# Kernel tuning notes

Measured on AMD Instinct MI355X. Metric: run time of the kernel, lower is better.

Reference implementation:

```python
import jax, jax.numpy as jnp
import numpy as np

N = 20000
E = 320000
HID = 256
NUM_RBF = 32
CUTOFF = 6.0
NUM_EDGE_TYPES = 2
LIGAND_NODE = 1
EPS = 1e-5

CENTERS = jnp.linspace(0.0, CUTOFF, NUM_RBF)  # [R]
GAMMA = 1.0 / max(float(CENTERS[1] - CENTERS[0]) ** 2, 1e-6)


def setup_inputs() -> dict:
    key = jax.random.key(0)
    ks = jax.random.split(key, 16)
    d = {}
    d['h'] = jax.random.normal(ks[0], (N, HID), dtype=jnp.float32)
    d['pos'] = jax.random.normal(ks[1], (N, 3), dtype=jnp.float32)
    d['edge_index'] = jax.random.randint(ks[2], (2, E), 0, N)
    d['edge_type'] = jax.random.randint(ks[3], (E,), 0, NUM_EDGE_TYPES)
    d['node_type'] = jax.random.randint(ks[4], (N,), 0, 2)
    s_in = 1.0 / np.sqrt(3 * HID + NUM_RBF)
    s_h = 1.0 / np.sqrt(HID)
    s_2h = 1.0 / np.sqrt(2 * HID)
    d['emb'] = jax.random.normal(ks[5], (NUM_EDGE_TYPES, HID), dtype=jnp.float32)
    d['W1m'] = jax.random.normal(ks[6], (3 * HID + NUM_RBF, HID), dtype=jnp.float32) * s_in
    d['b1m'] = jnp.zeros((HID,), dtype=jnp.float32)
    d['W2m'] = jax.random.normal(ks[7], (HID, HID), dtype=jnp.float32) * s_h
    d['b2m'] = jnp.zeros((HID,), dtype=jnp.float32)
    d['W1u'] = jax.random.normal(ks[8], (2 * HID, HID), dtype=jnp.float32) * s_2h
    d['b1u'] = jnp.zeros((HID,), dtype=jnp.float32)
    d['W2u'] = jax.random.normal(ks[9], (HID, HID), dtype=jnp.float32) * s_h
    d['b2u'] = jnp.zeros((HID,), dtype=jnp.float32)
    d['ln_g'] = jnp.ones((HID,), dtype=jnp.float32)
    d['ln_b'] = jnp.zeros((HID,), dtype=jnp.float32)
    return d


def _layernorm(x, g, b):
    mu = jnp.mean(x, axis=-1, keepdims=True)
    var = jnp.mean(jnp.square(x - mu), axis=-1, keepdims=True)
    return (x - mu) * jax.lax.rsqrt(var + EPS) * g + b


def reference(h, pos, edge_index, edge_type, node_type,
              emb, W1m, b1m, W2m, b2m, W1u, b1u, W2u, b2u, ln_g, ln_b):
    src, dst = edge_index[0], edge_index[1]
    rel = pos[src] - pos[dst]                      # [E,3]
    dist = jnp.linalg.norm(rel, axis=-1)           # [E]
    radial = jnp.exp(-GAMMA * jnp.square(dist[:, None] - CENTERS[None, :]))  # [E,R]
    edge_kind = emb[edge_type]                     # [E,H]
    m_in = jnp.concatenate([h[src], h[dst], edge_kind, radial], axis=-1)  # [E,3H+R]
    m = jax.nn.silu(m_in @ W1m + b1m)
    m_ij = jax.nn.silu(m @ W2m + b2m)              # [E,H] (dropout = identity in eval)
    seg_sum = jax.ops.segment_sum(m_ij, dst, num_segments=N)               # [N,H]
    cnt = jax.ops.segment_sum(jnp.ones((m_ij.shape[0],), m_ij.dtype), dst, num_segments=N)
    m_i = seg_sum / jnp.maximum(cnt, 1.0)[:, None]
    u = jax.nn.silu(jnp.concatenate([h, m_i], axis=-1) @ W1u + b1u)
    upd = u @ W2u + b2u                            # [N,H]
    lig = (node_type == LIGAND_NODE)[:, None]
    out = jnp.where(lig, _layernorm(h + upd, ln_g, ln_b), h)
    return out
```

## Files before the change

### kernel.cpp

```cpp
#include <hip/hip_runtime.h>
#include <hip/hip_fp16.h>
#include <math.h>

#define NN   20000
#define EE   320000
#define HID  256
#define GAMMA_C ((31.0f/6.0f)*(31.0f/6.0f))

typedef __attribute__((ext_vector_type(8)))  short    short8;
typedef __attribute__((ext_vector_type(8)))  _Float16 half8;
typedef __attribute__((ext_vector_type(16))) float    f32x16;

__device__ __forceinline__ float silu_f(float x) {
    return x / (1.0f + __expf(-x));
}

__device__ __forceinline__ short bf_hi(float x) {
    unsigned u = __float_as_uint(x);
    return (short)((u + 0x7fffu + ((u >> 16) & 1u)) >> 16);
}
__device__ __forceinline__ float bf_tof(short b) {
    return __uint_as_float(((unsigned)(unsigned short)b) << 16);
}
__device__ __forceinline__ void cvt_bf16_pair(float x, short* hi, short* lo) {
    short h = bf_hi(x);
    *hi = h;
    *lo = bf_hi(x - bf_tof(h));
}
__device__ __forceinline__ void cvt_f16_pair(float x, short* hi, short* lo) {
    __half h = __float2half_rn(x);
    *hi = (short)__half_as_ushort(h);
    *lo = (short)__half_as_ushort(__float2half_rn(x - __half2float(h)));
}
__device__ __forceinline__ short f16_bits(float x) {
    return (short)__half_as_ushort(__float2half_rn(x));
}

typedef __attribute__((address_space(1))) const void GV;
typedef __attribute__((address_space(3))) void LV;
__device__ __forceinline__ void gll16(const void* g, void* l) {
    __builtin_amdgcn_global_load_lds((GV*)g, (LV*)l, 16, 0, 0);
}

__device__ __forceinline__ short8 ldsfrag(const short* t, int row, int sg) {
    int s = sg ^ (row & 7);
    return *(const short8*)&t[row * 64 + s * 8];
}
__device__ __forceinline__ half8 ldsfragh(const short* t, int row, int sg) {
    int s = sg ^ (row & 7);
    return *(const half8*)&t[row * 64 + s * 8];
}

#define S0 (NN*HID)
#define S1 (2*HID)
#define S2 (256*800)
#define S3 (256*256)
#define S4 (256*512)
#define S5 (256*256)
#define PREP_TOTAL (S0+S1+S2+S3+S4+S5)

__global__ __launch_bounds__(256) void prep_all(
    const float* __restrict__ h, const float* __restrict__ emb,
    const float* __restrict__ W1m, const float* __restrict__ W2m,
    const float* __restrict__ W1u, const float* __restrict__ W2u,
    short* __restrict__ hpl, short* __restrict__ embpl,
    short* __restrict__ w1t, short* __restrict__ w2t,
    short* __restrict__ w1ut, short* __restrict__ w2ut)
{
    int i = blockIdx.x * 256 + threadIdx.x;
    float x; short *hi, *lo; int o; int f16 = 0;
    if (i < S0)              { x = h[i];   hi = hpl;   lo = hpl + S0;   o = i; }
    else if ((i -= S0) < S1) { x = emb[i]; hi = embpl; lo = embpl + S1; o = i; }
    else if ((i -= S1) < S2) { int n = i / 800, k = i - n * 800;
                               x = W1m[k * 256 + n]; hi = w1t; lo = w1t + S2; o = i; }
    else if ((i -= S2) < S3) { int n = i >> 8, k = i & 255;
                               x = W2m[k * 256 + n]; hi = w2t; lo = w2t + S3; o = i; f16 = 1; }
    else if ((i -= S3) < S4) { int n = i >> 9, k = i & 511;
                               x = W1u[k * 256 + n]; hi = w1ut; lo = w1ut + S4; o = i; }
    else if ((i -= S4) < S5) { int n = i >> 8, k = i & 255;
                               x = W2u[k * 256 + n]; hi = w2ut; lo = w2ut + S5; o = i; f16 = 1; }
    else return;
    short hb, lb;
    if (f16) cvt_f16_pair(x, &hb, &lb); else cvt_bf16_pair(x, &hb, &lb);
    hi[o] = hb; lo[o] = lb;
}

__global__ __launch_bounds__(512) void edge_mlp1(
    const short* __restrict__ hpl, const short* __restrict__ embpl,
    const short* __restrict__ w1t, const float* __restrict__ b1,
    const float* __restrict__ pos, const int* __restrict__ ei,
    const int* __restrict__ etype,
    short* __restrict__ mhi, float* __restrict__ cnt)
{
    __shared__ __align__(16) short At[128 * 64];
    __shared__ __align__(16) short Bt[256 * 64];
    __shared__ int srcS[128], dstS[128], etS[128];
    __shared__ float distS[128];

    const int tid = threadIdx.x, l = tid & 63, w = tid >> 6;
    const int e0 = blockIdx.x * 128;
    const int mh = w >> 2, ns = w & 3;

    if (tid < 128) {
        int s = ei[e0 + tid], d = ei[EE + e0 + tid];
        srcS[tid] = s; dstS[tid] = d; etS[tid] = etype[e0 + tid];
        float dx = pos[3*s]   - pos[3*d];
        float dy = pos[3*s+1] - pos[3*d+1];
        float dz = pos[3*s+2] - pos[3*d+2];
        distS[tid] = sqrtf(dx*dx + dy*dy + dz*dz);
        atomicAdd(&cnt[d], 1.0f);
    }
    __syncthreads();

    f32x16 acc[2][2];
    #pragma unroll
    for (int a = 0; a < 2; ++a)
        #pragma unroll
        for (int b = 0; b < 2; ++b)
            #pragma unroll
            for (int q = 0; q < 16; ++q) acc[a][b][q] = 0.0f;

    for (int c = 0; c < 25; ++c) {
        if (c < 24) {
            #pragma unroll
            for (int jj = 0; jj < 2; ++jj) {
                int j = w * 2 + jj;
                int row = j * 8 + (l >> 3), s = l & 7;
                int sg = s ^ (row & 7);
                int hl = sg >> 2, q = sg & 3;
                const short* gp;
                if (c < 8)
                    gp = hpl + (size_t)hl * (NN*HID) + (size_t)srcS[row] * HID + c*32 + q*8;
                else if (c < 16)
                    gp = hpl + (size_t)hl * (NN*HID) + (size_t)dstS[row] * HID + (c-8)*32 + q*8;
                else
                    gp = embpl + hl * (2*HID) + etS[row] * HID + (c-16)*32 + q*8;
                gll16(gp, &At[j * 512]);
            }
        } else {
            #pragma unroll
            for (int jj = 0; jj < 2; ++jj) {
                int it = tid * 2 + jj;
                int row = it >> 3, s = it & 7;
                int sg = s ^ (row & 7);
                int hl = sg >> 2, q = sg & 3;
                float d = distS[row];
                short8 v;
                #pragma unroll
                for (int k8 = 0; k8 < 8; ++k8) {
                    float cen = (float)(q * 8 + k8) * (6.0f / 31.0f);
                    float t = d - cen;
                    float f = __expf(-GAMMA_C * t * t);
                    short hb = bf_hi(f);
                    v[k8] = hl ? bf_hi(f - bf_tof(hb)) : hb;
                }
                *(short8*)&At[row * 64 + s * 8] = v;
            }
        }
        #pragma unroll
        for (int jj = 0; jj < 4; ++jj) {
            int j = w * 4 + jj;
            int n = j * 8 + (l >> 3), s = l & 7;
            int sg = s ^ (n & 7);
            int hl = sg >> 2, q = sg & 3;
            const short* gp = w1t + (size_t)hl * (256*800) + n * 800 + c*32 + q*8;
            gll16(gp, &Bt[j * 512]);
        }
        __syncthreads();
        #pragma unroll
        for (int t2 = 0; t2 < 2; ++t2) {
            short8 aF[2][2], bF[2][2];
            #pragma unroll
            for (int mf = 0; mf < 2; ++mf) {
                int row = mh * 64 + mf * 32 + (l & 31);
                #pragma unroll
                for (int hl = 0; hl < 2; ++hl)
                    aF[mf][hl] = ldsfrag(At, row, hl * 4 + t2 * 2 + (l >> 5));
            }
            #pragma unroll
            for (int nf = 0; nf < 2; ++nf) {
                int n = ns * 64 + nf * 32 + (l & 31);
                #pragma unroll
                for (int hl = 0; hl < 2; ++hl)
                    bF[nf][hl] = ldsfrag(Bt, n, hl * 4 + t2 * 2 + (l >> 5));
            }
            #pragma unroll
            for (int mf = 0; mf < 2; ++mf)
                #pragma unroll
                for (int nf = 0; nf < 2; ++nf) {
                    acc[mf][nf] = __builtin_amdgcn_mfma_f32_32x32x16_bf16(aF[mf][0], bF[nf][0], acc[mf][nf], 0, 0, 0);
                    acc[mf][nf] = __builtin_amdgcn_mfma_f32_32x32x16_bf16(aF[mf][0], bF[nf][1], acc[mf][nf], 0, 0, 0);
                    acc[mf][nf] = __builtin_amdgcn_mfma_f32_32x32x16_bf16(aF[mf][1], bF[nf][0], acc[mf][nf], 0, 0, 0);
                }
        }
        __syncthreads();
    }
    #pragma unroll
    for (int nf = 0; nf < 2; ++nf) {
        int col = ns * 64 + nf * 32 + (l & 31);
        float bb = b1[col];
        #pragma unroll
        for (int mf = 0; mf < 2; ++mf)
            #pragma unroll
            for (int r = 0; r < 16; ++r) {
                int row = mh * 64 + mf * 32 + (r & 3) + 8 * (r >> 2) + 4 * (l >> 5);
                float v = silu_f(acc[mf][nf][r] + bb);
                mhi[(size_t)(e0 + row) * HID + col] = f16_bits(v);
            }
    }
}

__global__ __launch_bounds__(512) void edge_mlp2(
    const short* __restrict__ mhi, const short* __restrict__ w2t,
    const float* __restrict__ b2, const int* __restrict__ ei,
    float* __restrict__ seg)
{
    __shared__ __align__(16) short Ah[128 * 64];
    __shared__ __align__(16) short Bh[256 * 64];
    __shared__ __align__(16) short Bl[256 * 64];
    __shared__ int dstS[128];
    const int tid = threadIdx.x, l = tid & 63, w = tid >> 6;
    const int e0 = blockIdx.x * 128;
    const int mh = w >> 2, ns = w & 3;
    if (tid < 128) dstS[tid] = ei[EE + e0 + tid];

    f32x16 acc[2][2];
    #pragma unroll
    for (int a = 0; a < 2; ++a)
        #pragma unroll
        for (int b = 0; b < 2; ++b)
            #pragma unroll
            for (int q = 0; q < 16; ++q) acc[a][b][q] = 0.0f;

    for (int c = 0; c < 4; ++c) {
        #pragma unroll
        for (int jj = 0; jj < 2; ++jj) {
            int j = w * 2 + jj;
            int row = j * 8 + (l >> 3), s = l & 7;
            int sg = s ^ (row & 7);
            gll16(mhi + (size_t)(e0 + row) * HID + c * 64 + sg * 8, &Ah[j * 512]);
        }
        #pragma unroll
        for (int jj = 0; jj < 8; ++jj) {
            int j = w * 8 + jj;
            int hf = j >> 5;
            int n = (j & 31) * 8 + (l >> 3), s = l & 7;
            int sg = s ^ (n & 7);
            const short* gp = w2t + (size_t)hf * (256*256) + n * HID + c * 64 + sg * 8;
            gll16(gp, hf ? &Bl[(j & 31) * 512] : &Bh[(j & 31) * 512]);
        }
        __syncthreads();
        #pragma unroll
        for (int t2 = 0; t2 < 4; ++t2) {
            int sg = t2 * 2 + (l >> 5);
            half8 aF[2], bH[2], bL[2];
            #pragma unroll
            for (int mf = 0; mf < 2; ++mf)
                aF[mf] = ldsfragh(Ah, mh * 64 + mf * 32 + (l & 31), sg);
            #pragma unroll
            for (int nf = 0; nf < 2; ++nf) {
                int n = ns * 64 + nf * 32 + (l & 31);
                bH[nf] = ldsfragh(Bh, n, sg);
                bL[nf] = ldsfragh(Bl, n, sg);
            }
            #pragma unroll
            for (int mf = 0; mf < 2; ++mf)
                #pragma unroll
                for (int nf = 0; nf < 2; ++nf) {
                    acc[mf][nf] = __builtin_amdgcn_mfma_f32_32x32x16_f16(aF[mf], bH[nf], acc[mf][nf], 0, 0, 0);
                    acc[mf][nf] = __builtin_amdgcn_mfma_f32_32x32x16_f16(aF[mf], bL[nf], acc[mf][nf], 0, 0, 0);
                }
        }
        __syncthreads();
    }
    #pragma unroll
    for (int nf = 0; nf < 2; ++nf) {
        int col = ns * 64 + nf * 32 + (l & 31);
        float bb = b2[col];
        #pragma unroll
        for (int mf = 0; mf < 2; ++mf)
            #pragma unroll
            for (int r = 0; r < 16; ++r) {
                int row = mh * 64 + mf * 32 + (r & 3) + 8 * (r >> 2) + 4 * (l >> 5);
                float v = silu_f(acc[mf][nf][r] + bb);
                atomicAdd(&seg[(size_t)dstS[row] * HID + col], v);
            }
    }
}

__global__ __launch_bounds__(256) void mi_prep(
    const float* __restrict__ seg, const float* __restrict__ cnt,
    short* __restrict__ mipl)
{
    int i = blockIdx.x * 256 + threadIdx.x;
    int row = i >> 8;
    float v = seg[i] / fmaxf(cnt[row], 1.0f);
    short hb, lb;
    cvt_bf16_pair(v, &hb, &lb);
    mipl[i] = hb;
    mipl[(size_t)NN * HID + i] = lb;
}

__global__ __launch_bounds__(512) void node_mlp1(
    const short* __restrict__ hpl, const short* __restrict__ mipl,
    const short* __restrict__ w1ut, const float* __restrict__ b1,
    short* __restrict__ u)
{
    __shared__ __align__(16) short At[128 * 64];
    __shared__ __align__(16) short Bt[256 * 64];
    const int tid = threadIdx.x, l = tid & 63, w = tid >> 6;
    const int n0 = blockIdx.x * 128;
    const int mh = w >> 2, ns = w & 3;

    f32x16 acc[2][2];
    #pragma unroll
    for (int a = 0; a < 2; ++a)
        #pragma unroll
        for (int b = 0; b < 2; ++b)
            #pragma unroll
            for (int q = 0; q < 16; ++q) acc[a][b][q] = 0.0f;

    for (int c = 0; c < 16; ++c) {
        #pragma unroll
        for (int jj = 0; jj < 2; ++jj) {
            int j = w * 2 + jj;
            int row = j * 8 + (l >> 3), s = l & 7;
            int sg = s ^ (row & 7);
            int hl = sg >> 2, q = sg & 3;
            int node = min(n0 + row, NN - 1);
            const short* gp = (c < 8)
                ? hpl  + (size_t)hl * (NN*HID) + (size_t)node * HID + c * 32 + q * 8
                : mipl + (size_t)hl * (NN*HID) + (size_t)node * HID + (c - 8) * 32 + q * 8;
            gll16(gp, &At[j * 512]);
        }
        #pragma unroll
        for (int jj = 0; jj < 4; ++jj) {
            int j = w * 4 + jj;
            int n = j * 8 + (l >> 3), s = l & 7;
            int sg = s ^ (n & 7);
            int hl = sg >> 2, q = sg & 3;
            const short* gp = w1ut + (size_t)hl * (256*512) + n * 512 + c * 32 + q * 8;
            gll16(gp, &Bt[j * 512]);
        }
        __syncthreads();
        #pragma unroll
        for (int t2 = 0; t2 < 2; ++t2) {
            short8 aF[2][2], bF[2][2];
            #pragma unroll
            for (int mf = 0; mf < 2; ++mf) {
                int row = mh * 64 + mf * 32 + (l & 31);
                #pragma unroll
                for (int hl = 0; hl < 2; ++hl)
                    aF[mf][hl] = ldsfrag(At, row, hl * 4 + t2 * 2 + (l >> 5));
            }
            #pragma unroll
            for (int nf = 0; nf < 2; ++nf) {
                int n = ns * 64 + nf * 32 + (l & 31);
                #pragma unroll
                for (int hl = 0; hl < 2; ++hl)
                    bF[nf][hl] = ldsfrag(Bt, n, hl * 4 + t2 * 2 + (l >> 5));
            }
            #pragma unroll
            for (int mf = 0; mf < 2; ++mf)
                #pragma unroll
                for (int nf = 0; nf < 2; ++nf) {
                    acc[mf][nf] = __builtin_amdgcn_mfma_f32_32x32x16_bf16(aF[mf][0], bF[nf][0], acc[mf][nf], 0, 0, 0);
                    acc[mf][nf] = __builtin_amdgcn_mfma_f32_32x32x16_bf16(aF[mf][0], bF[nf][1], acc[mf][nf], 0, 0, 0);
                    acc[mf][nf] = __builtin_amdgcn_mfma_f32_32x32x16_bf16(aF[mf][1], bF[nf][0], acc[mf][nf], 0, 0, 0);
                }
        }
        __syncthreads();
    }
    #pragma unroll
    for (int nf = 0; nf < 2; ++nf) {
        int col = ns * 64 + nf * 32 + (l & 31);
        float bb = b1[col];
        #pragma unroll
        for (int mf = 0; mf < 2; ++mf)
            #pragma unroll
            for (int r = 0; r < 16; ++r) {
                int row = mh * 64 + mf * 32 + (r & 3) + 8 * (r >> 2) + 4 * (l >> 5);
                if (n0 + row < NN) {
                    float v = silu_f(acc[mf][nf][r] + bb);
                    u[(size_t)(n0 + row) * HID + col] = f16_bits(v);
                }
            }
    }
}

__global__ __launch_bounds__(512) void node_mlp2(
    const short* __restrict__ u, const short* __restrict__ w2ut,
    const float* __restrict__ b2, const float* __restrict__ h,
    const int* __restrict__ ntype, const float* __restrict__ lng,
    const float* __restrict__ lnb, float* __restrict__ out)
{
    __shared__ __align__(16) short Ah[128 * 64];
    __shared__ __align__(16) short Bh[256 * 64];
    __shared__ __align__(16) short Bl[256 * 64];
    __shared__ float red1[4][128], red2[4][128];
    __shared__ float muS[128], rsS[128];
    const int tid = threadIdx.x, l = tid & 63, w = tid >> 6;
    const int n0 = blockIdx.x * 128;
    const int mh = w >> 2, ns = w & 3;

    f32x16 acc[2][2];
    #pragma unroll
    for (int a = 0; a < 2; ++a)
        #pragma unroll
        for (int b = 0; b < 2; ++b)
            #pragma unroll
            for (int q = 0; q < 16; ++q) acc[a][b][q] = 0.0f;

    for (int c = 0; c < 4; ++c) {
        #pragma unroll
        for (int jj = 0; jj < 2; ++jj) {
            int j = w * 2 + jj;
            int row = j * 8 + (l >> 3), s = l & 7;
            int sg = s ^ (row & 7);
            int node = min(n0 + row, NN - 1);
            gll16(u + (size_t)node * HID + c * 64 + sg * 8, &Ah[j * 512]);
        }
        #pragma unroll
        for (int jj = 0; jj < 8; ++jj) {
            int j = w * 8 + jj;
            int hf = j >> 5;
            int n = (j & 31) * 8 + (l >> 3), s = l & 7;
            int sg = s ^ (n & 7);
            const short* gp = w2ut + (size_t)hf * (256*256) + n * HID + c * 64 + sg * 8;
            gll16(gp, hf ? &Bl[(j & 31) * 512] : &Bh[(j & 31) * 512]);
        }
        __syncthreads();
        #pragma unroll
        for (int t2 = 0; t2 < 4; ++t2) {
            int sg = t2 * 2 + (l >> 5);
            half8 aF[2], bH[2], bL[2];
            #pragma unroll
            for (int mf = 0; mf < 2; ++mf)
                aF[mf] = ldsfragh(Ah, mh * 64 + mf * 32 + (l & 31), sg);
            #pragma unroll
            for (int nf = 0; nf < 2; ++nf) {
                int n = ns * 64 + nf * 32 + (l & 31);
                bH[nf] = ldsfragh(Bh, n, sg);
                bL[nf] = ldsfragh(Bl, n, sg);
            }
            #pragma unroll
            for (int mf = 0; mf < 2; ++mf)
                #pragma unroll
                for (int nf = 0; nf < 2; ++nf) {
                    acc[mf][nf] = __builtin_amdgcn_mfma_f32_32x32x16_f16(aF[mf], bH[nf], acc[mf][nf], 0, 0, 0);
                    acc[mf][nf] = __builtin_amdgcn_mfma_f32_32x32x16_f16(aF[mf], bL[nf], acc[mf][nf], 0, 0, 0);
                }
        }
        __syncthreads();
    }

    #pragma unroll
    for (int nf = 0; nf < 2; ++nf) {
        int col = ns * 64 + nf * 32 + (l & 31);
        float bb = b2[col];
        #pragma unroll
        for (int mf = 0; mf < 2; ++mf)
            #pragma unroll
            for (int r = 0; r < 16; ++r) {
                int row = mh * 64 + mf * 32 + (r & 3) + 8 * (r >> 2) + 4 * (l >> 5);
                int node = min(n0 + row, NN - 1);
                acc[mf][nf][r] += bb + h[(size_t)node * HID + col];
            }
    }
    #pragma unroll
    for (int mf = 0; mf < 2; ++mf)
        #pragma unroll
        for (int r = 0; r < 16; ++r) {
            float v1 = acc[mf][0][r] + acc[mf][1][r];
            float v2 = acc[mf][0][r]*acc[mf][0][r] + acc[mf][1][r]*acc[mf][1][r];
            #pragma unroll
            for (int off = 16; off >= 1; off >>= 1) {
                v1 += __shfl_xor(v1, off, 64);
                v2 += __shfl_xor(v2, off, 64);
            }
            if ((l & 31) == 0) {
                int row = mh * 64 + mf * 32 + (r & 3) + 8 * (r >> 2) + 4 * (l >> 5);
                red1[ns][row] = v1; red2[ns][row] = v2;
            }
        }
    __syncthreads();
    if (tid < 128) {
        float s1 = red1[0][tid] + red1[1][tid] + red1[2][tid] + red1[3][tid];
        float s2 = red2[0][tid] + red2[1][tid] + red2[2][tid] + red2[3][tid];
        float mu = s1 * (1.0f / 256.0f);
        float var = s2 * (1.0f / 256.0f) - mu * mu;
        muS[tid] = mu;
        rsS[tid] = rsqrtf(var + 1e-5f);
    }
    __syncthreads();
    #pragma unroll
    for (int nf = 0; nf < 2; ++nf) {
        int col = ns * 64 + nf * 32 + (l & 31);
        float g = lng[col], bt = lnb[col];
        #pragma unroll
        for (int mf = 0; mf < 2; ++mf)
            #pragma unroll
            for (int r = 0; r < 16; ++r) {
                int row = mh * 64 + mf * 32 + (r & 3) + 8 * (r >> 2) + 4 * (l >> 5);
                int node = n0 + row;
                if (node < NN) {
                    float y;
                    if (ntype[node] == 1)
                        y = (acc[mf][nf][r] - muS[row]) * rsS[row] * g + bt;
                    else
                        y = h[(size_t)node * HID + col];
                    out[(size_t)node * HID + col] = y;
                }
            }
    }
}

#define SWZ(k, e) ((e) ^ ((((k) >> 2) & 7) << 2))

__global__ __launch_bounds__(256) void edge_fp32(
    const float* __restrict__ h, const float* __restrict__ pos,
    const int* __restrict__ ei, const int* __restrict__ etype,
    const float* __restrict__ emb,
    const float* __restrict__ W1, const float* __restrict__ b1,
    const float* __restrict__ W2, const float* __restrict__ b2,
    float* __restrict__ seg, float* __restrict__ cnt)
{
    __shared__ float A1T[16][32];
    __shared__ float Bt[16][256];
    __shared__ float A2T[256][32];
    __shared__ float distS[32];
    __shared__ int   srcS[32], dstS[32], etS[32];
    const int tid = threadIdx.x;
    const int e0  = blockIdx.x * 32;
    if (tid < 32) {
        const int e = e0 + tid;
        const int s = ei[e];
        const int d = ei[EE + e];
        srcS[tid] = s; dstS[tid] = d; etS[tid] = etype[e];
        const float dx = pos[3*s+0] - pos[3*d+0];
        const float dy = pos[3*s+1] - pos[3*d+1];
        const float dz = pos[3*s+2] - pos[3*d+2];
        distS[tid] = sqrtf(dx*dx + dy*dy + dz*dz);
        atomicAdd(&cnt[d], 1.0f);
    }
    __syncthreads();
    const int c0 = (tid & 63) * 4;
    const int r0 = (tid >> 6) * 8;
    float acc[8][4];
    #pragma unroll
    for (int i = 0; i < 8; ++i)
        #pragma unroll
        for (int j = 0; j < 4; ++j) acc[i][j] = 0.0f;
    const float step  = 6.0f / 31.0f;
    for (int k0 = 0; k0 < 800; k0 += 16) {
        if (tid < 128) {
            const int e = tid >> 2;
            const int q = (tid & 3) * 4;
            const int k = k0 + q;
            float4 v;
            if (k < 256)       v = *(const float4*)&h[(size_t)srcS[e]*HID + k];
            else if (k < 512)  v = *(const float4*)&h[(size_t)dstS[e]*HID + (k - 256)];
            else if (k < 768)  v = *(const float4*)&emb[(size_t)etS[e]*HID + (k - 512)];
            else {
                const float de = distS[e];
                const float t0 = de - step*(float)(k-768);
                const float t1 = de - step*(float)(k-767);
                const float t2 = de - step*(float)(k-766);
                const float t3 = de - step*(float)(k-765);
                v = make_float4(__expf(-GAMMA_C*t0*t0), __expf(-GAMMA_C*t1*t1),
                                __expf(-GAMMA_C*t2*t2), __expf(-GAMMA_C*t3*t3));
            }
            A1T[q+0][e] = v.x; A1T[q+1][e] = v.y;
            A1T[q+2][e] = v.z; A1T[q+3][e] = v.w;
        }
        #pragma unroll
        for (int p = 0; p < 4; ++p) {
            const int idx = p*256 + tid;
            const int k   = idx >> 6;
            const int n   = (idx & 63) * 4;
            *(float4*)&Bt[k][n] = *(const float4*)&W1[(size_t)(k0+k)*HID + n];
        }
        __syncthreads();
        #pragma unroll
        for (int kk = 0; kk < 16; ++kk) {
            const float4 b  = *(const float4*)&Bt[kk][c0];
            const float4 a0 = *(const float4*)&A1T[kk][r0];
            const float4 a1 = *(const float4*)&A1T[kk][r0+4];
            const float a[8] = {a0.x,a0.y,a0.z,a0.w,a1.x,a1.y,a1.z,a1.w};
            #pragma unroll
            for (int i = 0; i < 8; ++i) {
                acc[i][0] = fmaf(a[i], b.x, acc[i][0]);
                acc[i][1] = fmaf(a[i], b.y, acc[i][1]);
                acc[i][2] = fmaf(a[i], b.z, acc[i][2]);
                acc[i][3] = fmaf(a[i], b.w, acc[i][3]);
            }
        }
        __syncthreads();
    }
    {
        const float4 b1v = *(const float4*)&b1[c0];
        const float bb[4] = {b1v.x, b1v.y, b1v.z, b1v.w};
        #pragma unroll
        for (int j = 0; j < 4; ++j) {
            const int k = c0 + j;
            #pragma unroll
            for (int i = 0; i < 8; ++i) {
                const float x = acc[i][j] + bb[j];
                A2T[k][SWZ(k, r0+i)] = silu_f(x);
                acc[i][j] = 0.0f;
            }
        }
    }
    __syncthreads();
    for (int k0 = 0; k0 < HID; k0 += 16) {
        #pragma unroll
        for (int p = 0; p < 4; ++p) {
            const int idx = p*256 + tid;
            const int k   = idx >> 6;
            const int n   = (idx & 63) * 4;
            *(float4*)&Bt[k][n] = *(const float4*)&W2[(size_t)(k0+k)*HID + n];
        }
        __syncthreads();
        #pragma unroll
        for (int kk = 0; kk < 16; ++kk) {
            const int K = k0 + kk;
            const float4 b  = *(const float4*)&Bt[kk][c0];
            const float4 a0 = *(const float4*)&A2T[K][SWZ(K, r0)];
            const float4 a1 = *(const float4*)&A2T[K][SWZ(K, r0+4)];
            const float a[8] = {a0.x,a0.y,a0.z,a0.w,a1.x,a1.y,a1.z,a1.w};
            #pragma unroll
            for (int i = 0; i < 8; ++i) {
                acc[i][0] = fmaf(a[i], b.x, acc[i][0]);
                acc[i][1] = fmaf(a[i], b.y, acc[i][1]);
                acc[i][2] = fmaf(a[i], b.z, acc[i][2]);
                acc[i][3] = fmaf(a[i], b.w, acc[i][3]);
            }
        }
        __syncthreads();
    }
    {
        const float4 b2v = *(const float4*)&b2[c0];
        const float bb[4] = {b2v.x, b2v.y, b2v.z, b2v.w};
        #pragma unroll
        for (int i = 0; i < 8; ++i) {
            const int d = dstS[r0 + i];
            float* outp = &seg[(size_t)d*HID + c0];
            #pragma unroll
            for (int j = 0; j < 4; ++j) {
                const float x = acc[i][j] + bb[j];
                atomicAdd(&outp[j], silu_f(x));
            }
        }
    }
}

__global__ __launch_bounds__(256) void node_fp32(
    const float* __restrict__ h, const float* __restrict__ seg,
    const float* __restrict__ cnt, const int* __restrict__ ntype,
    const float* __restrict__ W1, const float* __restrict__ b1,
    const float* __restrict__ W2, const float* __restrict__ b2,
    const float* __restrict__ lng, const float* __restrict__ lnb,
    float* __restrict__ out)
{
    __shared__ float A1T[16][32];
    __shared__ float Bt[16][256];
    __shared__ float A2T[256][32];
    __shared__ float invS[32];
    const int tid = threadIdx.x;
    const int n0  = blockIdx.x * 32;
    if (tid < 32) invS[tid] = 1.0f / fmaxf(cnt[n0 + tid], 1.0f);
    __syncthreads();
    const int c0 = (tid & 63) * 4;
    const int r0 = (tid >> 6) * 8;
    float acc[8][4];
    #pragma unroll
    for (int i = 0; i < 8; ++i)
        #pragma unroll
        for (int j = 0; j < 4; ++j) acc[i][j] = 0.0f;
    for (int k0 = 0; k0 < 512; k0 += 16) {
        if (tid < 128) {
            const int e = tid >> 2;
            const int q = (tid & 3) * 4;
            const int k = k0 + q;
            float4 v;
            if (k < 256) v = *(const float4*)&h[(size_t)(n0+e)*HID + k];
            else {
                v = *(const float4*)&seg[(size_t)(n0+e)*HID + (k - 256)];
                const float ic = invS[e];
                v.x *= ic; v.y *= ic; v.z *= ic; v.w *= ic;
            }
            A1T[q+0][e] = v.x; A1T[q+1][e] = v.y;
            A1T[q+2][e] = v.z; A1T[q+3][e] = v.w;
        }
        #pragma unroll
        for (int p = 0; p < 4; ++p) {
            const int idx = p*256 + tid;
            const int k   = idx >> 6;
            const int n   = (idx & 63) * 4;
            *(float4*)&Bt[k][n] = *(const float4*)&W1[(size_t)(k0+k)*HID + n];
        }
        __syncthreads();
        #pragma unroll
        for (int kk = 0; kk < 16; ++kk) {
            const float4 b  = *(const float4*)&Bt[kk][c0];
            const float4 a0 = *(const float4*)&A1T[kk][r0];
            const float4 a1 = *(const float4*)&A1T[kk][r0+4];
            const float a[8] = {a0.x,a0.y,a0.z,a0.w,a1.x,a1.y,a1.z,a1.w};
            #pragma unroll
            for (int i = 0; i < 8; ++i) {
                acc[i][0] = fmaf(a[i], b.x, acc[i][0]);
                acc[i][1] = fmaf(a[i], b.y, acc[i][1]);
                acc[i][2] = fmaf(a[i], b.z, acc[i][2]);
                acc[i][3] = fmaf(a[i], b.w, acc[i][3]);
            }
        }
        __syncthreads();
    }
    {
        const float4 b1v = *(const float4*)&b1[c0];
        const float bb[4] = {b1v.x, b1v.y, b1v.z, b1v.w};
        #pragma unroll
        for (int j = 0; j < 4; ++j) {
            const int k = c0 + j;
            #pragma unroll
            for (int i = 0; i < 8; ++i) {
                const float x = acc[i][j] + bb[j];
                A2T[k][SWZ(k, r0+i)] = silu_f(x);
                acc[i][j] = 0.0f;
            }
        }
    }
    __syncthreads();
    for (int k0 = 0; k0 < HID; k0 += 16) {
        #pragma unroll
        for (int p = 0; p < 4; ++p) {
            const int idx = p*256 + tid;
            const int k   = idx >> 6;
            const int n   = (idx & 63) * 4;
            *(float4*)&Bt[k][n] = *(const float4*)&W2[(size_t)(k0+k)*HID + n];
        }
        __syncthreads();
        #pragma unroll
        for (int kk = 0; kk < 16; ++kk) {
            const int K = k0 + kk;
            const float4 b  = *(const float4*)&Bt[kk][c0];
            const float4 a0 = *(const float4*)&A2T[K][SWZ(K, r0)];
            const float4 a1 = *(const float4*)&A2T[K][SWZ(K, r0+4)];
            const float a[8] = {a0.x,a0.y,a0.z,a0.w,a1.x,a1.y,a1.z,a1.w};
            #pragma unroll
            for (int i = 0; i < 8; ++i) {
                acc[i][0] = fmaf(a[i], b.x, acc[i][0]);
                acc[i][1] = fmaf(a[i], b.y, acc[i][1]);
                acc[i][2] = fmaf(a[i], b.z, acc[i][2]);
                acc[i][3] = fmaf(a[i], b.w, acc[i][3]);
            }
        }
        __syncthreads();
    }
    {
        const float4 b2v = *(const float4*)&b2[c0];
        const float bb[4] = {b2v.x, b2v.y, b2v.z, b2v.w};
        float4 hv[8];
        #pragma unroll
        for (int i = 0; i < 8; ++i) {
            hv[i] = *(const float4*)&h[(size_t)(n0+r0+i)*HID + c0];
            acc[i][0] = hv[i].x + acc[i][0] + bb[0];
            acc[i][1] = hv[i].y + acc[i][1] + bb[1];
            acc[i][2] = hv[i].z + acc[i][2] + bb[2];
            acc[i][3] = hv[i].w + acc[i][3] + bb[3];
        }
        float s1[8], s2[8];
        #pragma unroll
        for (int i = 0; i < 8; ++i) {
            s1[i] = acc[i][0] + acc[i][1] + acc[i][2] + acc[i][3];
            s2[i] = acc[i][0]*acc[i][0] + acc[i][1]*acc[i][1]
                  + acc[i][2]*acc[i][2] + acc[i][3]*acc[i][3];
        }
        #pragma unroll
        for (int off = 32; off >= 1; off >>= 1) {
            #pragma unroll
            for (int i = 0; i < 8; ++i) {
                s1[i] += __shfl_xor(s1[i], off, 64);
                s2[i] += __shfl_xor(s2[i], off, 64);
            }
        }
        const float4 gv = *(const float4*)&lng[c0];
        const float4 bv = *(const float4*)&lnb[c0];
        const float g[4] = {gv.x, gv.y, gv.z, gv.w};
        const float bb2[4] = {bv.x, bv.y, bv.z, bv.w};
        #pragma unroll
        for (int i = 0; i < 8; ++i) {
            const int n = n0 + r0 + i;
            const bool lig = (ntype[n] == 1);
            float4 y;
            if (lig) {
                const float mu  = s1[i] * (1.0f/256.0f);
                const float var = s2[i] * (1.0f/256.0f) - mu*mu;
                const float rs  = rsqrtf(var + 1e-5f);
                y.x = (acc[i][0] - mu) * rs * g[0] + bb2[0];
                y.y = (acc[i][1] - mu) * rs * g[1] + bb2[1];
                y.z = (acc[i][2] - mu) * rs * g[2] + bb2[2];
                y.w = (acc[i][3] - mu) * rs * g[3] + bb2[3];
            } else {
                y = hv[i];
            }
            *(float4*)&out[(size_t)n*HID + c0] = y;
        }
    }
}

extern "C" void kernel_launch(void* const* d_in, const int* in_sizes, int n_in,
                              void* d_out, int out_size, void* d_ws, size_t ws_size,
                              hipStream_t stream) {
    (void)in_sizes; (void)n_in; (void)out_size;
    const float* h    = (const float*)d_in[0];
    const float* pos  = (const float*)d_in[1];
    const int*   ei   = (const int*)  d_in[2];
    const int*   et   = (const int*)  d_in[3];
    const int*   nt   = (const int*)  d_in[4];
    const float* emb  = (const float*)d_in[5];
    const float* W1m  = (const float*)d_in[6];
    const float* b1m  = (const float*)d_in[7];
    const float* W2m  = (const float*)d_in[8];
    const float* b2m  = (const float*)d_in[9];
    const float* W1u  = (const float*)d_in[10];
    const float* b1u  = (const float*)d_in[11];
    const float* W2u  = (const float*)d_in[12];
    const float* b2u  = (const float*)d_in[13];
    const float* lng  = (const float*)d_in[14];
    const float* lnb  = (const float*)d_in[15];
    float* out = (float*)d_out;

    size_t o = 0;
    auto al = [&](size_t b) { size_t r = o; o = (o + b + 511) & ~(size_t)511; return r; };
    const size_t o_seg  = al((size_t)NN * HID * 4);
    const size_t o_cnt  = al((size_t)NN * 4);
    const size_t o_zend = o;
    const size_t o_hpl  = al((size_t)2 * NN * HID * 2);
    const size_t o_emb  = al((size_t)2 * 2 * HID * 2);
    const size_t o_w1t  = al((size_t)2 * 256 * 800 * 2);
    const size_t o_w2t  = al((size_t)2 * 256 * 256 * 2);
    const size_t o_w1ut = al((size_t)2 * 256 * 512 * 2);
    const size_t o_w2ut = al((size_t)2 * 256 * 256 * 2);
    const size_t o_mipl = al((size_t)2 * NN * HID * 2);
    const size_t o_upl  = al((size_t)NN * HID * 2);
    const size_t o_mhi  = al((size_t)EE * HID * 2);
    const size_t need = o;

    char* ws = (char*)d_ws;
    float* seg = (float*)(ws + o_seg);
    float* cnt = (float*)(ws + o_cnt);

    if (ws_size >= need) {
        short* hpl   = (short*)(ws + o_hpl);
        short* embpl = (short*)(ws + o_emb);
        short* w1t   = (short*)(ws + o_w1t);
        short* w2t   = (short*)(ws + o_w2t);
        short* w1ut  = (short*)(ws + o_w1ut);
        short* w2ut  = (short*)(ws + o_w2ut);
        short* mipl  = (short*)(ws + o_mipl);
        short* upl   = (short*)(ws + o_upl);
        short* mhi   = (short*)(ws + o_mhi);

        hipMemsetAsync(d_ws, 0, o_zend, stream);
        prep_all<<<PREP_TOTAL / 256, 256, 0, stream>>>(
            h, emb, W1m, W2m, W1u, W2u, hpl, embpl, w1t, w2t, w1ut, w2ut);
        edge_mlp1<<<EE / 128, 512, 0, stream>>>(
            hpl, embpl, w1t, b1m, pos, ei, et, mhi, cnt);
        edge_mlp2<<<EE / 128, 512, 0, stream>>>(mhi, w2t, b2m, ei, seg);
        mi_prep<<<(NN * HID) / 256, 256, 0, stream>>>(seg, cnt, mipl);
        const int nb = (NN + 127) / 128;
        node_mlp1<<<nb, 512, 0, stream>>>(hpl, mipl, w1ut, b1u, upl);
        node_mlp2<<<nb, 512, 0, stream>>>(upl, w2ut, b2u, h, nt, lng, lnb, out);
    } else {
        hipMemsetAsync(d_ws, 0, ((size_t)NN * HID + NN) * sizeof(float), stream);
        float* seg0 = (float*)d_ws;
        float* cnt0 = seg0 + (size_t)NN * HID;
        edge_fp32<<<EE / 32, 256, 0, stream>>>(h, pos, ei, et, emb,
                                               W1m, b1m, W2m, b2m, seg0, cnt0);
        node_fp32<<<NN / 32, 256, 0, stream>>>(h, seg0, cnt0, nt,
                                               W1u, b1u, W2u, b2u, lng, lnb, out);
    }
}
```

Baseline: 1.015 ms.

## Split edge MLP output columns across grid and double-buffer LDS tiles

Both edge MLP kernels now split the 256 output columns into two 128-column halves via blockIdx.y, which doubles the number of blocks. Each block keeps smaller LDS tiles, double-buffered so the next K-chunk is loaded while the current one feeds the MFMAs. Launch bounds request 4 blocks per CU to raise occupancy and hide gather latency. In exchange, the gathered A rows (h[src], h[dst], emb, and the radial features) are loaded and computed twice, once per column half.

```diff
diff --git a/kernel.cpp b/kernel.cpp
--- a/kernel.cpp
+++ b/kernel.cpp
@@ -45,6 +45,14 @@
 __device__ __forceinline__ short8 ldsfrag(const short* t, int row, int sg) {
     int s = sg ^ (row & 7);
     return *(const short8*)&t[row * 64 + s * 8];
+}
+__device__ __forceinline__ half8 ldsfragh32(const short* t, int row, int sg) {
+    int s = sg ^ (row & 3);
+    return *(const half8*)&t[row * 32 + s * 8];
+}
+__device__ __forceinline__ short8 ldsfrag32(const short* t, int row, int sg) {
+    int s = sg ^ (row & 3);
+    return *(const short8*)&t[row * 32 + s * 8];
 }
 __device__ __forceinline__ half8 ldsfragh(const short* t, int row, int sg) {
     int s = sg ^ (row & 7);
@@ -85,20 +93,21 @@
     hi[o] = hb; lo[o] = lb;
 }
 
-__global__ __launch_bounds__(512) void edge_mlp1(
+__global__ __launch_bounds__(512, 4) void edge_mlp1(
     const short* __restrict__ hpl, const short* __restrict__ embpl,
     const short* __restrict__ w1t, const float* __restrict__ b1,
     const float* __restrict__ pos, const int* __restrict__ ei,
     const int* __restrict__ etype,
     short* __restrict__ mhi, float* __restrict__ cnt)
 {
-    __shared__ __align__(16) short At[128 * 64];
-    __shared__ __align__(16) short Bt[256 * 64];
+    __shared__ __align__(16) short At[2][128 * 64];
+    __shared__ __align__(16) short Bt[2][128 * 64];
     __shared__ int srcS[128], dstS[128], etS[128];
     __shared__ float distS[128];
 
     const int tid = threadIdx.x, l = tid & 63, w = tid >> 6;
     const int e0 = blockIdx.x * 128;
+    const int cb = blockIdx.y;
     const int mh = w >> 2, ns = w & 3;
 
     if (tid < 128) {
@@ -108,19 +117,11 @@
         float dy = pos[3*s+1] - pos[3*d+1];
         float dz = pos[3*s+2] - pos[3*d+2];
         distS[tid] = sqrtf(dx*dx + dy*dy + dz*dz);
-        atomicAdd(&cnt[d], 1.0f);
+        if (cb == 0) atomicAdd(&cnt[d], 1.0f);
     }
     __syncthreads();
 
-    f32x16 acc[2][2];
-    #pragma unroll
-    for (int a = 0; a < 2; ++a)
-        #pragma unroll
-        for (int b = 0; b < 2; ++b)
-            #pragma unroll
-            for (int q = 0; q < 16; ++q) acc[a][b][q] = 0.0f;
-
-    for (int c = 0; c < 25; ++c) {
+    auto stageA = [&](int buf, int c) {
         if (c < 24) {
             #pragma unroll
             for (int jj = 0; jj < 2; ++jj) {
@@ -135,7 +136,7 @@
                     gp = hpl + (size_t)hl * (NN*HID) + (size_t)dstS[row] * HID + (c-8)*32 + q*8;
                 else
                     gp = embpl + hl * (2*HID) + etS[row] * HID + (c-16)*32 + q*8;
-                gll16(gp, &At[j * 512]);
+                gll16(gp, &At[buf][j * 512]);
             }
         } else {
             #pragma unroll
@@ -154,135 +155,153 @@
                     short hb = bf_hi(f);
                     v[k8] = hl ? bf_hi(f - bf_tof(hb)) : hb;
                 }
-                *(short8*)&At[row * 64 + s * 8] = v;
-            }
-        }
-        #pragma unroll
-        for (int jj = 0; jj < 4; ++jj) {
-            int j = w * 4 + jj;
+                *(short8*)&At[buf][row * 64 + s * 8] = v;
+            }
+        }
+    };
+    auto stageB = [&](int buf, int c) {
+        #pragma unroll
+        for (int jj = 0; jj < 2; ++jj) {
+            int j = w * 2 + jj;
             int n = j * 8 + (l >> 3), s = l & 7;
             int sg = s ^ (n & 7);
             int hl = sg >> 2, q = sg & 3;
-            const short* gp = w1t + (size_t)hl * (256*800) + n * 800 + c*32 + q*8;
-            gll16(gp, &Bt[j * 512]);
-        }
-        __syncthreads();
+            const short* gp = w1t + (size_t)hl * (256*800)
+                            + (size_t)(cb*128 + n) * 800 + c*32 + q*8;
+            gll16(gp, &Bt[buf][j * 512]);
+        }
+    };
+
+    f32x16 acc[2];
+    #pragma unroll
+    for (int a = 0; a < 2; ++a)
+        #pragma unroll
+        for (int q = 0; q < 16; ++q) acc[a][q] = 0.0f;
+
+    stageA(0, 0); stageB(0, 0);
+    __syncthreads();
+
+    int cur = 0;
+    for (int c = 0; c < 25; ++c) {
+        if (c < 24) { stageA(cur ^ 1, c + 1); stageB(cur ^ 1, c + 1); }
         #pragma unroll
         for (int t2 = 0; t2 < 2; ++t2) {
-            short8 aF[2][2], bF[2][2];
+            short8 aF[2][2], bF[2];
             #pragma unroll
             for (int mf = 0; mf < 2; ++mf) {
                 int row = mh * 64 + mf * 32 + (l & 31);
                 #pragma unroll
                 for (int hl = 0; hl < 2; ++hl)
-                    aF[mf][hl] = ldsfrag(At, row, hl * 4 + t2 * 2 + (l >> 5));
-            }
-            #pragma unroll
-            for (int nf = 0; nf < 2; ++nf) {
-                int n = ns * 64 + nf * 32 + (l & 31);
+                    aF[mf][hl] = ldsfrag(&At[cur][0], row, hl * 4 + t2 * 2 + (l >> 5));
+            }
+            {
+                int n = ns * 32 + (l & 31);
                 #pragma unroll
                 for (int hl = 0; hl < 2; ++hl)
-                    bF[nf][hl] = ldsfrag(Bt, n, hl * 4 + t2 * 2 + (l >> 5));
-            }
-            #pragma unroll
-            for (int mf = 0; mf < 2; ++mf)
-                #pragma unroll
-                for (int nf = 0; nf < 2; ++nf) {
-                    acc[mf][nf] = __builtin_amdgcn_mfma_f32_32x32x16_bf16(aF[mf][0], bF[nf][0], acc[mf][nf], 0, 0, 0);
-                    acc[mf][nf] = __builtin_amdgcn_mfma_f32_32x32x16_bf16(aF[mf][0], bF[nf][1], acc[mf][nf], 0, 0, 0);
-                    acc[mf][nf] = __builtin_amdgcn_mfma_f32_32x32x16_bf16(aF[mf][1], bF[nf][0], acc[mf][nf], 0, 0, 0);
-                }
-        }
-        __syncthreads();
-    }
-    #pragma unroll
-    for (int nf = 0; nf < 2; ++nf) {
-        int col = ns * 64 + nf * 32 + (l & 31);
+                    bF[hl] = ldsfrag(&Bt[cur][0], n, hl * 4 + t2 * 2 + (l >> 5));
+            }
+            #pragma unroll
+            for (int mf = 0; mf < 2; ++mf) {
+                acc[mf] = __builtin_amdgcn_mfma_f32_32x32x16_bf16(aF[mf][0], bF[0], acc[mf], 0, 0, 0);
+                acc[mf] = __builtin_amdgcn_mfma_f32_32x32x16_bf16(aF[mf][0], bF[1], acc[mf], 0, 0, 0);
+                acc[mf] = __builtin_amdgcn_mfma_f32_32x32x16_bf16(aF[mf][1], bF[0], acc[mf], 0, 0, 0);
+            }
+        }
+        __syncthreads();
+        cur ^= 1;
+    }
+
+    {
+        int col = cb * 128 + ns * 32 + (l & 31);
         float bb = b1[col];
         #pragma unroll
         for (int mf = 0; mf < 2; ++mf)
             #pragma unroll
             for (int r = 0; r < 16; ++r) {
                 int row = mh * 64 + mf * 32 + (r & 3) + 8 * (r >> 2) + 4 * (l >> 5);
-                float v = silu_f(acc[mf][nf][r] + bb);
+                float v = silu_f(acc[mf][r] + bb);
                 mhi[(size_t)(e0 + row) * HID + col] = f16_bits(v);
             }
     }
 }
 
-__global__ __launch_bounds__(512) void edge_mlp2(
+__global__ __launch_bounds__(512, 4) void edge_mlp2(
     const short* __restrict__ mhi, const short* __restrict__ w2t,
     const float* __restrict__ b2, const int* __restrict__ ei,
     float* __restrict__ seg)
 {
-    __shared__ __align__(16) short Ah[128 * 64];
-    __shared__ __align__(16) short Bh[256 * 64];
-    __shared__ __align__(16) short Bl[256 * 64];
+    __shared__ __align__(16) short Ah[2][128 * 32];
+    __shared__ __align__(16) short Bh[2][128 * 32];
+    __shared__ __align__(16) short Bl[2][128 * 32];
     __shared__ int dstS[128];
     const int tid = threadIdx.x, l = tid & 63, w = tid >> 6;
     const int e0 = blockIdx.x * 128;
+    const int cb = blockIdx.y;
     const int mh = w >> 2, ns = w & 3;
     if (tid < 128) dstS[tid] = ei[EE + e0 + tid];
-
-    f32x16 acc[2][2];
+    __syncthreads();
+
+    auto stageA = [&](int buf, int c) {
+        int row = w * 16 + (l >> 2), s = l & 3;
+        int sg = s ^ (row & 3);
+        gll16(mhi + (size_t)(e0 + row) * HID + c * 32 + sg * 8, &Ah[buf][w * 512]);
+    };
+    auto stageB = [&](int buf, int c) {
+        #pragma unroll
+        for (int jj = 0; jj < 2; ++jj) {
+            int j = w * 2 + jj;
+            int hf = j >> 3, jn = j & 7;
+            int n = jn * 16 + (l >> 2), s = l & 3;
+            int sg = s ^ (n & 3);
+            const short* gp = w2t + (size_t)hf * (256*256)
+                            + (size_t)(cb*128 + n) * HID + c * 32 + sg * 8;
+            gll16(gp, hf ? &Bl[buf][jn * 512] : &Bh[buf][jn * 512]);
+        }
+    };
+
+    f32x16 acc[2];
     #pragma unroll
     for (int a = 0; a < 2; ++a)
         #pragma unroll
-        for (int b = 0; b < 2; ++b)
-            #pragma unroll
-            for (int q = 0; q < 16; ++q) acc[a][b][q] = 0.0f;
-
-    for (int c = 0; c < 4; ++c) {
-        #pragma unroll
-        for (int jj = 0; jj < 2; ++jj) {
-            int j = w * 2 + jj;
-            int row = j * 8 + (l >> 3), s = l & 7;
-            int sg = s ^ (row & 7);
-            gll16(mhi + (size_t)(e0 + row) * HID + c * 64 + sg * 8, &Ah[j * 512]);
-        }
-        #pragma unroll
-        for (int jj = 0; jj < 8; ++jj) {
-            int j = w * 8 + jj;
-            int hf = j >> 5;
-            int n = (j & 31) * 8 + (l >> 3), s = l & 7;
-            int sg = s ^ (n & 7);
-            const short* gp = w2t + (size_t)hf * (256*256) + n * HID + c * 64 + sg * 8;
-            gll16(gp, hf ? &Bl[(j & 31) * 512] : &Bh[(j & 31) * 512]);
-        }
-        __syncthreads();
-        #pragma unroll
-        for (int t2 = 0; t2 < 4; ++t2) {
+        for (int q = 0; q < 16; ++q) acc[a][q] = 0.0f;
+
+    stageA(0, 0); stageB(0, 0);
+    __syncthreads();
+
+    int cur = 0;
+    for (int c = 0; c < 8; ++c) {
+        if (c < 7) { stageA(cur ^ 1, c + 1); stageB(cur ^ 1, c + 1); }
+        #pragma unroll
+        for (int t2 = 0; t2 < 2; ++t2) {
             int sg = t2 * 2 + (l >> 5);
-            half8 aF[2], bH[2], bL[2];
+            half8 aF[2], bH, bL;
             #pragma unroll
             for (int mf = 0; mf < 2; ++mf)
-                aF[mf] = ldsfragh(Ah, mh * 64 + mf * 32 + (l & 31), sg);
-            #pragma unroll
-            for (int nf = 0; nf < 2; ++nf) {
-                int n = ns * 64 + nf * 32 + (l & 31);
-                bH[nf] = ldsfragh(Bh, n, sg);
-                bL[nf] = ldsfragh(Bl, n, sg);
-            }
-            #pragma unroll
-            for (int mf = 0; mf < 2; ++mf)
-                #pragma unroll
-                for (int nf = 0; nf < 2; ++nf) {
-                    acc[mf][nf] = __builtin_amdgcn_mfma_f32_32x32x16_f16(aF[mf], bH[nf], acc[mf][nf], 0, 0, 0);
-                    acc[mf][nf] = __builtin_amdgcn_mfma_f32_32x32x16_f16(aF[mf], bL[nf], acc[mf][nf], 0, 0, 0);
-                }
-        }
-        __syncthreads();
-    }
-    #pragma unroll
-    for (int nf = 0; nf < 2; ++nf) {
-        int col = ns * 64 + nf * 32 + (l & 31);
+                aF[mf] = ldsfragh32(&Ah[cur][0], mh * 64 + mf * 32 + (l & 31), sg);
+            {
+                int n = ns * 32 + (l & 31);
+                bH = ldsfragh32(&Bh[cur][0], n, sg);
+                bL = ldsfragh32(&Bl[cur][0], n, sg);
+            }
+            #pragma unroll
+            for (int mf = 0; mf < 2; ++mf) {
+                acc[mf] = __builtin_amdgcn_mfma_f32_32x32x16_f16(aF[mf], bH, acc[mf], 0, 0, 0);
+                acc[mf] = __builtin_amdgcn_mfma_f32_32x32x16_f16(aF[mf], bL, acc[mf], 0, 0, 0);
+            }
+        }
+        __syncthreads();
+        cur ^= 1;
+    }
+
+    {
+        int col = cb * 128 + ns * 32 + (l & 31);
         float bb = b2[col];
         #pragma unroll
         for (int mf = 0; mf < 2; ++mf)
             #pragma unroll
             for (int r = 0; r < 16; ++r) {
                 int row = mh * 64 + mf * 32 + (r & 3) + 8 * (r >> 2) + 4 * (l >> 5);
-                float v = silu_f(acc[mf][nf][r] + bb);
+                float v = silu_f(acc[mf][r] + bb);
                 atomicAdd(&seg[(size_t)dstS[row] * HID + col], v);
             }
     }
@@ -865,9 +884,9 @@
         hipMemsetAsync(d_ws, 0, o_zend, stream);
         prep_all<<<PREP_TOTAL / 256, 256, 0, stream>>>(
             h, emb, W1m, W2m, W1u, W2u, hpl, embpl, w1t, w2t, w1ut, w2ut);
-        edge_mlp1<<<EE / 128, 512, 0, stream>>>(
+        edge_mlp1<<<dim3(EE / 128, 2), 512, 0, stream>>>(
             hpl, embpl, w1t, b1m, pos, ei, et, mhi, cnt);
-        edge_mlp2<<<EE / 128, 512, 0, stream>>>(mhi, w2t, b2m, ei, seg);
+        edge_mlp2<<<dim3(EE / 128, 2), 512, 0, stream>>>(mhi, w2t, b2m, ei, seg);
         mi_prep<<<(NN * HID) / 256, 256, 0, stream>>>(seg, cnt, mipl);
         const int nb = (NN + 127) / 128;
         node_mlp1<<<nb, 512, 0, stream>>>(hpl, mipl, w1ut, b1u, upl);
```

Result: faster. 935.8 us (-7.8%).
